# Kernel tuning notes

Measured on AMD Instinct MI355X. Metric: run time of the kernel, lower is better.

The kernel has to match this reference:

```python
import jax, jax.numpy as jnp
import numpy as np

N, E, F_IN, D_COORD, W, KW, KIN, DEPTH = 10000, 300000, 3, 3, 32, 256, 6, 4

def _lin(k, i, o):
    return jax.random.normal(k, (i, o), jnp.float32) * (1.0 / np.sqrt(i))

def setup_inputs() -> dict:
    key = jax.random.key(0)
    ks = jax.random.split(key, 16)
    x = jax.random.normal(ks[0], (N, F_IN), jnp.float32)
    edge_index = jax.random.randint(ks[1], (2, E), 0, N, jnp.int64)
    edge_attr = jax.random.normal(ks[2], (E, KIN), jnp.float32)
    coords_init = jax.random.normal(ks[3], (N, D_COORD), jnp.float32)
    return {
        "x": x, "edge_index": edge_index, "edge_attr": edge_attr,
        "coords_init": coords_init,
        "fc1_w": _lin(ks[4], F_IN, W), "fc1_b": jnp.zeros((W,), jnp.float32),
        # kernel DenseNet: [ker_in, ker_width//2, ker_width, width**2]
        "ker1_w": _lin(ks[5], KIN, KW // 2), "ker1_b": jnp.zeros((KW // 2,), jnp.float32),
        "ker2_w": _lin(ks[6], KW // 2, KW), "ker2_b": jnp.zeros((KW,), jnp.float32),
        "ker3_w": _lin(ks[7], KW, W * W), "ker3_b": jnp.zeros((W * W,), jnp.float32),
        # coord MLP: Linear(W,W)+ReLU+Linear(W,1)
        "cm1_w": _lin(ks[8], W, W), "cm1_b": jnp.zeros((W,), jnp.float32),
        "cm2_w": _lin(ks[9], W, 1), "cm2_b": jnp.zeros((1,), jnp.float32),
        # fc2: Linear(W,2W)+ReLU+Linear(2W,1)
        "fc2a_w": _lin(ks[10], W, 2 * W), "fc2a_b": jnp.zeros((2 * W,), jnp.float32),
        "fc2b_w": _lin(ks[11], 2 * W, 1), "fc2b_b": jnp.zeros((1,), jnp.float32),
        "depth": DEPTH,
    }

def reference(x, edge_index, edge_attr, coords_init,
              fc1_w, fc1_b, ker1_w, ker1_b, ker2_w, ker2_b, ker3_w, ker3_b,
              cm1_w, cm1_b, cm2_w, cm2_b, fc2a_w, fc2a_b, fc2b_w, fc2b_b, depth):
    n = x.shape[0]
    w = fc1_w.shape[1]
    row, col = edge_index[0], edge_index[1]
    h = x @ fc1_w + fc1_b  # [N, W]
    # edge kernel MLP -> per-edge [W, W] matrix (edge_attr fixed across layers)
    k = jax.nn.relu(edge_attr @ ker1_w + ker1_b)
    k = jax.nn.relu(k @ ker2_w + ker2_b)
    k = (k @ ker3_w + ker3_b).reshape(-1, w, w)  # [E, W, W]
    cnt = jnp.clip(jax.ops.segment_sum(jnp.ones((row.shape[0], 1), h.dtype), row, n), 1.0)
    coord = coords_init
    for _ in range(depth):
        m = jnp.einsum('eij,ej->ei', k, h[col])              # gather + kernel apply
        agg = jax.ops.segment_sum(m, row, n) / cnt           # mean scatter to nodes
        we = jax.nn.relu(m @ cm1_w + cm1_b) @ cm2_w + cm2_b  # [E, 1] coord weights
        trans = (coord[row] - coord[col]) * we               # equivariant edge vectors
        coord = coord + jax.ops.segment_sum(trans, row, n) / cnt
        h = jax.nn.relu(h + agg)
    out = jax.nn.relu(h @ fc2a_w + fc2a_b) @ fc2b_w + fc2b_b  # [N, 1]
    return out, coord
```

## Files before the change

kernel.cpp:

```cpp
#include <hip/hip_runtime.h>

#define NN 10000
#define NE 300000
#define DEPTH 4

typedef unsigned int   u32;
typedef unsigned short u16;
typedef unsigned char  u8;

typedef _Float16 half8  __attribute__((ext_vector_type(8)));
typedef _Float16 half2t __attribute__((ext_vector_type(2)));
typedef float  floatx16 __attribute__((ext_vector_type(16)));

__device__ __forceinline__ u32 f2h(float f) {
    f = fminf(fmaxf(f, -60000.f), 60000.f);
    _Float16 h = (_Float16)f;
    return (u32)__builtin_bit_cast(u16, h);
}
__device__ __forceinline__ float h2f(u16 b) {
    return (float)__builtin_bit_cast(_Float16, b);
}
__device__ __forceinline__ u32 pkrtz2(float a, float b) {
    return __builtin_bit_cast(u32, __builtin_amdgcn_cvt_pkrtz(a, b));
}
__device__ __forceinline__ u32 dq2(u32 x, u32 sel) {
    const half2t h1024 = {(_Float16)1024.f, (_Float16)1024.f};
    half2t v = __builtin_bit_cast(half2t, __builtin_amdgcn_perm(x, 0x64646464u, sel));
    return __builtin_bit_cast(u32, v - h1024);
}

__global__ void sentinel_kernel(float* out, int n, float val) {
    int i = blockIdx.x * 256 + threadIdx.x;
    if (i < n) out[i] = val;
}

__global__ void detect_idx_kernel(const int* __restrict__ ei, int* __restrict__ flag) {
    __shared__ int nz;
    if (threadIdx.x == 0) nz = 0;
    __syncthreads();
    if (ei[threadIdx.x * 2 + 1] != 0) atomicAdd(&nz, 1);
    __syncthreads();
    if (threadIdx.x == 0) *flag = (nz == 0) ? 1 : 0;
}

__global__ __launch_bounds__(256) void convert_idx_kernel(
    const int* __restrict__ ei, const int* __restrict__ flag,
    int* __restrict__ ridx, int* __restrict__ cidx)
{
    int e = blockIdx.x * 256 + threadIdx.x;
    if (e >= 2 * NE) return;
    const int is64 = *flag;
    int v = is64 ? ei[2 * e] : ei[e];
    if (e < NE) ridx[e] = v; else cidx[e - NE] = v;
}

__global__ __launch_bounds__(256) void init_nodes_kernel(
    const float* __restrict__ x, const float* __restrict__ fc1w,
    const float* __restrict__ fc1b, const float* __restrict__ ci,
    float* __restrict__ h, float* __restrict__ coord)
{
    int idx = blockIdx.x * 256 + threadIdx.x;
    if (idx < NN * 32) {
        int v = idx >> 5, f = idx & 31;
        float acc = fc1b[f];
#pragma unroll
        for (int i = 0; i < 3; i++) acc += x[v * 3 + i] * fc1w[i * 32 + f];
        h[idx] = acc;
    }
    if (idx < NN * 3) coord[idx] = ci[idx];
}

__global__ __launch_bounds__(256) void count_kernel(
    const int* __restrict__ ridx, const int* __restrict__ cidx,
    int* __restrict__ rowcnt, int* __restrict__ colcnt)
{
    int e = blockIdx.x * 256 + threadIdx.x;
    if (e < NE) { atomicAdd(&rowcnt[ridx[e]], 1); atomicAdd(&colcnt[cidx[e]], 1); }
}

__global__ void scan_kernel(const int* __restrict__ colcnt, const int* __restrict__ rowcnt,
                            int* __restrict__ cstart, int* __restrict__ cnext,
                            int* __restrict__ rstart, int* __restrict__ rnext,
                            float* __restrict__ invc, int mode)
{
    __shared__ int partC[256], partR[256];
    const int t = threadIdx.x;
    int sumC = 0, sumR = 0;
    for (int i = 0; i < 40; i++) {
        int v = t * 40 + i;
        if (v < NN) { sumC += colcnt[v]; sumR += rowcnt[v]; }
    }
    partC[t] = sumC; partR[t] = sumR;
    __syncthreads();
    if (t == 0) {
        int rc = 0, rr = 0;
        for (int i = 0; i < 256; i++) {
            int tc = partC[i]; partC[i] = rc; rc += tc;
            int tr = partR[i]; partR[i] = rr; rr += tr;
        }
    }
    __syncthreads();
    int runC = partC[t], runR = partR[t];
    for (int i = 0; i < 40; i++) {
        int v = t * 40 + i;
        if (v < NN) {
            cstart[v] = runC; cnext[v] = runC; runC += colcnt[v];
            if (mode) { rstart[v] = runR; rnext[v] = runR; runR += rowcnt[v]; }
        }
    }
    if (t == 255) { cstart[NN] = runC; if (mode) rstart[NN] = runR; }
    for (int v = t; v < NN; v += 256) invc[v] = 1.0f / fmaxf((float)rowcnt[v], 1.0f);
}

__global__ __launch_bounds__(256) void scatter_kernel(
    const int* __restrict__ cidx, const int* __restrict__ ridx,
    int* __restrict__ cnext, int* __restrict__ rnext,
    int* __restrict__ elist, int* __restrict__ rpos, int* __restrict__ rcol,
    int mode)
{
    int e = blockIdx.x * 256 + threadIdx.x;
    if (e >= NE) return;
    int pos = atomicAdd(&cnext[cidx[e]], 1);
    elist[pos] = e;
    if (mode) {
        int rp = atomicAdd(&rnext[ridx[e]], 1);
        rpos[e] = rp;
        rcol[rp] = cidx[e];
    }
}

__global__ __launch_bounds__(256) void w2pack_kernel(
    const float* __restrict__ w2, u16* __restrict__ w2h)
{
    const int slot = blockIdx.x * 256 + threadIdx.x;
    const int c = slot >> 9, s = (slot >> 6) & 7, l = slot & 63;
    const int li = l & 31, hf = l >> 5;
    const int k0 = s * 16 + hf * 8, col = c * 32 + li;
    u32 pk[8];
#pragma unroll
    for (int j = 0; j < 8; j++) pk[j] = f2h(w2[(size_t)(k0 + j) * 256 + col]);
    uint4 o;
    o.x = pk[0] | (pk[1] << 16);
    o.y = pk[2] | (pk[3] << 16);
    o.z = pk[4] | (pk[5] << 16);
    o.w = pk[6] | (pk[7] << 16);
    *(uint4*)&w2h[(size_t)slot * 8] = o;
}

__global__ void cm1pack_kernel(const float* __restrict__ cm1w, u16* __restrict__ cmpk)
{
    const int t = threadIdx.x;
    if (t >= 128) return;
    const int s2 = t >> 6, l = t & 63, li = l & 31, hf = l >> 5;
    u32 pk[8];
#pragma unroll
    for (int j = 0; j < 8; j++) pk[j] = f2h(cm1w[(s2 * 16 + hf * 8 + j) * 32 + li]);
    uint4 o;
    o.x = pk[0] | (pk[1] << 16);
    o.y = pk[2] | (pk[3] << 16);
    o.z = pk[4] | (pk[5] << 16);
    o.w = pk[6] | (pk[7] << 16);
    *(uint4*)&cmpk[(size_t)(s2 * 64 + l) * 8] = o;
}

__global__ __launch_bounds__(256) void w3pack_kernel(
    const float* __restrict__ w3, u16* __restrict__ w3g)
{
    const int slot = blockIdx.x * 256 + threadIdx.x;
    const int lane = slot & 63;
    const int ks   = (slot >> 6) & 1;
    const int pt   = slot >> 7;
    const int p    = pt * 32 + (lane & 31);
    const int kb   = ks * 16 + (lane >> 5) * 8;
    const int s  = p >> 9;
    const int hf = (p >> 8) & 1;
    const int i  = (p >> 3) & 31;
    const int j7 = p & 7;
    const int c  = s * 16 + hf * 8 + j7;
    const float* wp = &w3[(size_t)c * 1024 + i * 32 + kb];
    const float4 x0 = *(const float4*)wp;
    const float4 x1 = *(const float4*)(wp + 4);
    uint4 o;
    o.x = f2h(x0.x) | (f2h(x0.y) << 16);
    o.y = f2h(x0.z) | (f2h(x0.w) << 16);
    o.z = f2h(x1.x) | (f2h(x1.y) << 16);
    o.w = f2h(x1.z) | (f2h(x1.w) << 16);
    *(uint4*)&w3g[(size_t)slot * 8] = o;
}

__global__ __launch_bounds__(256, 4) void mlp_k2_kernel(
    const float* __restrict__ ea,
    const float* __restrict__ w1, const float* __restrict__ b1,
    const u16* __restrict__ w2h, const float* __restrict__ b2,
    u8* __restrict__ k2base, u16* __restrict__ k2s)
{
    __shared__ __align__(16) float ea_s[32 * 6];
    __shared__ __align__(16) u16   k1f[4096];
    __shared__ __align__(16) u16   M_s[32 * 258];
    __shared__ float pmax_s[4][32];
    const int t  = threadIdx.x;
    const int e0 = blockIdx.x * 32;

    for (int idx = t; idx < 192; idx += 256)
        ea_s[idx] = ea[(size_t)e0 * 6 + idx];
    __syncthreads();

    for (int slot = t; slot < 512; slot += 256) {
        const int s  = slot >> 6;
        const int l  = slot & 63;
        const int li = l & 31, hf = l >> 5;
        const int k0 = s * 16 + hf * 8;
        float acc[8];
        {
            const float4 ba = *(const float4*)&b1[k0];
            const float4 bb = *(const float4*)&b1[k0 + 4];
            acc[0] = ba.x; acc[1] = ba.y; acc[2] = ba.z; acc[3] = ba.w;
            acc[4] = bb.x; acc[5] = bb.y; acc[6] = bb.z; acc[7] = bb.w;
        }
#pragma unroll
        for (int i = 0; i < 6; i++) {
            const float ev = ea_s[li * 6 + i];
            const float4 wa = *(const float4*)&w1[i * 128 + k0];
            const float4 wb = *(const float4*)&w1[i * 128 + k0 + 4];
            acc[0] += ev * wa.x; acc[1] += ev * wa.y;
            acc[2] += ev * wa.z; acc[3] += ev * wa.w;
            acc[4] += ev * wb.x; acc[5] += ev * wb.y;
            acc[6] += ev * wb.z; acc[7] += ev * wb.w;
        }
        uint4 o;
        o.x = pkrtz2(fmaxf(acc[0], 0.f), fmaxf(acc[1], 0.f));
        o.y = pkrtz2(fmaxf(acc[2], 0.f), fmaxf(acc[3], 0.f));
        o.z = pkrtz2(fmaxf(acc[4], 0.f), fmaxf(acc[5], 0.f));
        o.w = pkrtz2(fmaxf(acc[6], 0.f), fmaxf(acc[7], 0.f));
        *(uint4*)&k1f[slot * 8] = o;
    }
    __syncthreads();

    {
        const int w  = t >> 6, l = t & 63;
        const int li = l & 31, hf = l >> 5;
#pragma unroll
        for (int ct = 0; ct < 2; ct++) {
            const int c = w * 2 + ct;
            floatx16 acc;
#pragma unroll
            for (int r = 0; r < 16; r++) acc[r] = 0.f;
#pragma unroll
            for (int s = 0; s < 8; s++) {
                const half8 a = __builtin_bit_cast(half8,
                    *(const uint4*)&k1f[(s * 64 + l) * 8]);
                const half8 b = __builtin_bit_cast(half8,
                    *(const uint4*)&w2h[(((size_t)c * 8 + s) * 64 + l) * 8]);
                acc = __builtin_amdgcn_mfma_f32_32x32x16_f16(a, b, acc, 0, 0, 0);
            }
            const float bb = b2[c * 32 + li];
#pragma unroll
            for (int r = 0; r < 16; r++) {
                const int e = (r & 3) + 8 * (r >> 2) + 4 * hf;
                M_s[e * 258 + c * 32 + li] =
                    __builtin_bit_cast(u16, (_Float16)fmaxf(acc[r] + bb, 0.f));
            }
        }
    }
    __syncthreads();

    {
        const int el = t & 31, qq = t >> 5;
        const int w  = t >> 6;
        u32 hw[16];
#pragma unroll
        for (int c = 0; c < 16; c++)
            hw[c] = *(const u32*)&M_s[el * 258 + qq * 32 + c * 2];

        half2t pm = __builtin_bit_cast(half2t, hw[0]);
#pragma unroll
        for (int c = 1; c < 16; c++)
            pm = __builtin_elementwise_max(pm, __builtin_bit_cast(half2t, hw[c]));
        float mx = fmaxf((float)pm[0], (float)pm[1]);
        mx = fmaxf(mx, __shfl_xor(mx, 32, 64));
        if ((t & 32) == 0) pmax_s[w][el] = mx;
        __syncthreads();
        mx = fmaxf(fmaxf(pmax_s[0][el], pmax_s[1][el]),
                   fmaxf(pmax_s[2][el], pmax_s[3][el]));
        const float sc  = mx / 255.f;
        const float inv = (mx > 0.f) ? 255.f / mx : 0.f;
        if (t < 32) k2s[e0 + el] = (u16)f2h(sc);
        const float magic = 8388608.f;
        u32 w8[8];
#pragma unroll
        for (int u = 0; u < 8; u++) {
            const u32 a = hw[u * 2], b = hw[u * 2 + 1];
            const float v0 = h2f((u16)a);
            const float v1 = h2f((u16)(a >> 16));
            const float v2 = h2f((u16)b);
            const float v3 = h2f((u16)(b >> 16));
            const u32 r0 = __builtin_bit_cast(u32, fmaf(v0, inv, magic));
            const u32 r1 = __builtin_bit_cast(u32, fmaf(v1, inv, magic));
            const u32 r2 = __builtin_bit_cast(u32, fmaf(v2, inv, magic));
            const u32 r3 = __builtin_bit_cast(u32, fmaf(v3, inv, magic));
            const u32 p01 = __builtin_amdgcn_perm(r1, r0, 0x0C0C0400u);
            const u32 p23 = __builtin_amdgcn_perm(r3, r2, 0x0C0C0400u);
            w8[u] = __builtin_amdgcn_perm(p23, p01, 0x05040100u);
        }
        u8* outp = k2base + (size_t)(e0 + el) * 256 + qq * 32;
        *(uint4*)outp        = make_uint4(w8[0], w8[1], w8[2], w8[3]);
        *(uint4*)(outp + 16) = make_uint4(w8[4], w8[5], w8[6], w8[7]);
    }
}

__global__ __launch_bounds__(256) void g_kernel(
    const float* __restrict__ h, const u16* __restrict__ w3g,
    u16* __restrict__ Gg)
{
    const int t = threadIdx.x, w = t >> 6, l = t & 63;
    const int li = l & 31, hf = l >> 5;
    const int n0 = blockIdx.x * 32;
    const int node = n0 + li;

    half8 a0, a1;
    if (node < NN) {
        const float* hp = &h[(size_t)node * 32 + hf * 8];
        const float4 x0 = *(const float4*)hp;
        const float4 x1 = *(const float4*)(hp + 4);
        const float4 y0 = *(const float4*)(hp + 16);
        const float4 y1 = *(const float4*)(hp + 20);
        uint4 ua, ub;
        ua.x = pkrtz2(x0.x, x0.y); ua.y = pkrtz2(x0.z, x0.w);
        ua.z = pkrtz2(x1.x, x1.y); ua.w = pkrtz2(x1.z, x1.w);
        ub.x = pkrtz2(y0.x, y0.y); ub.y = pkrtz2(y0.z, y0.w);
        ub.z = pkrtz2(y1.x, y1.y); ub.w = pkrtz2(y1.z, y1.w);
        a0 = __builtin_bit_cast(half8, ua);
        a1 = __builtin_bit_cast(half8, ub);
    } else {
        const uint4 z = make_uint4(0u, 0u, 0u, 0u);
        a0 = __builtin_bit_cast(half8, z);
        a1 = __builtin_bit_cast(half8, z);
    }

    const int pt0 = blockIdx.y * 64 + w * 16;
    const int full = (n0 + 32 <= NN) ? 1 : 0;
#pragma unroll 4
    for (int it = 0; it < 16; it++) {
        const int pt = pt0 + it;
        const uint4 b0u = *(const uint4*)&w3g[((size_t)pt * 2 + 0) * 512 + (size_t)l * 8];
        const uint4 b1u = *(const uint4*)&w3g[((size_t)pt * 2 + 1) * 512 + (size_t)l * 8];
        floatx16 acc;
#pragma unroll
        for (int r = 0; r < 16; r++) acc[r] = 0.f;
        acc = __builtin_amdgcn_mfma_f32_32x32x16_f16(
            a0, __builtin_bit_cast(half8, b0u), acc, 0, 0, 0);
        acc = __builtin_amdgcn_mfma_f32_32x32x16_f16(
            a1, __builtin_bit_cast(half8, b1u), acc, 0, 0, 0);
        if (full) {
#pragma unroll
            for (int r = 0; r < 16; r++) {
                const int nn = n0 + (r & 3) + 8 * (r >> 2) + 4 * hf;
                Gg[(size_t)nn * 8192 + pt * 32 + li] = (u16)f2h(acc[r]);
            }
        } else {
#pragma unroll
            for (int r = 0; r < 16; r++) {
                const int nn = n0 + (r & 3) + 8 * (r >> 2) + 4 * hf;
                if (nn < NN)
                    Gg[(size_t)nn * 8192 + pt * 32 + li] = (u16)f2h(acc[r]);
            }
        }
    }
}

__global__ __launch_bounds__(256, 3) void edge_kernel(
    const int* __restrict__ cstart, const int* __restrict__ elist,
    const int* __restrict__ ridx, const int* __restrict__ rpos,
    const u8* __restrict__ k2base, const u16* __restrict__ k2s,
    const u16* __restrict__ Gg, const float* __restrict__ coord,
    const u16* __restrict__ cmpk, const float* __restrict__ cm1b,
    const float* __restrict__ cm2w, const float* __restrict__ cm2b,
    const float* __restrict__ h, const float* __restrict__ b3,
    float* __restrict__ agg, float* __restrict__ dco,
    u16* __restrict__ mbuf, u16* __restrict__ webuf, int mode)
{
    const int t    = threadIdx.x;
    const int w    = t >> 6;
    const int l    = t & 63;
    const int li   = l & 31;
    const int half = l >> 5;

    __shared__ __align__(16) float Mlds_all[4][32 * 34];
    __shared__ int   idxS_all[4][32];
    __shared__ float seS_all[4][32];
    float* Mlds = Mlds_all[w];
    int*   idxS = idxS_all[w];
    float* seS  = seS_all[w];

    const int n = blockIdx.x * 4 + w;
    if (n >= NN) return;
    const int s0  = cstart[n];
    const int deg = cstart[n + 1] - s0;
    if (deg == 0) return;

    half8 cmb[2];
    cmb[0] = __builtin_bit_cast(half8, *(const uint4*)&cmpk[(size_t)(0 * 64 + l) * 8]);
    cmb[1] = __builtin_bit_cast(half8, *(const uint4*)&cmpk[(size_t)(1 * 64 + l) * 8]);
    half8 onesb;
#pragma unroll
    for (int j = 0; j < 8; j++) onesb[j] = (_Float16)1.0f;
    const float cm1bq = cm1b[li];
    const float cm2q  = cm2w[li];
    const float cm2b0 = cm2b[0];
    float bv = 0.f;
    {
        const float* hn = &h[(size_t)n * 32];
        const float* bp = &b3[(size_t)li * 32];
#pragma unroll
        for (int c2 = 0; c2 < 8; c2++) {
            const float4 hv = *(const float4*)&hn[c2 * 4];
            const float4 bq = *(const float4*)&bp[c2 * 4];
            bv += hv.x * bq.x + hv.y * bq.y + hv.z * bq.z + hv.w * bq.w;
        }
    }
    const float con   = (mode == 0 && li < 3) ? coord[(size_t)n * 3 + li] : 0.f;
    const u16* Gn = Gg + (size_t)n * 8192;

    for (int base = 0; base < deg; base += 32) {
        const int mye   = base + li;
        const int valid = (mye < deg) ? 1 : 0;
        const int eid   = valid ? elist[s0 + mye] : 0;
        const float se  = valid ? h2f(k2s[eid]) : 0.f;
        if (l < 32) { idxS[l] = valid ? (mode ? rpos[eid] : ridx[eid]) : 0; seS[l] = se; }

        uint4 gr[16];
#pragma unroll
        for (int s = 0; s < 16; s++)
            gr[s] = *(const uint4*)(Gn + s * 512 + l * 8);
        const u8* k2row = k2base + (size_t)eid * 256 + half * 8;
        uint2 kr[16];
#pragma unroll
        for (int s = 0; s < 16; s++) kr[s] = *(const uint2*)(k2row + s * 16);

        floatx16 acc;
#pragma unroll
        for (int r = 0; r < 16; r++) acc[r] = 0.f;
#pragma unroll
        for (int s = 0; s < 16; s++) {
            uint4 au;
            au.x = dq2(kr[s].x, 0x00050004u);
            au.y = dq2(kr[s].x, 0x00070006u);
            au.z = dq2(kr[s].y, 0x00050004u);
            au.w = dq2(kr[s].y, 0x00070006u);
            acc = __builtin_amdgcn_mfma_f32_32x32x16_f16(
                __builtin_bit_cast(half8, au),
                __builtin_bit_cast(half8, gr[s]), acc, 0, 0, 0);
        }
#pragma unroll
        for (int r = 0; r < 16; r++) {
            const int e = (r & 3) + 8 * (r >> 2) + 4 * half;
            acc[r] = acc[r] * seS[e] + bv;
        }

#pragma unroll
        for (int r = 0; r < 16; r++) {
            const int e = (r & 3) + 8 * (r >> 2) + 4 * half;
            Mlds[e * 34 + li] = acc[r];
        }
        if (mode == 0) {
#pragma unroll
            for (int r = 0; r < 16; r++) {
                const int e = (r & 3) + 8 * (r >> 2) + 4 * half;
                if (base + e < deg)
                    atomicAdd(&agg[(size_t)idxS[e] * 32 + li], acc[r]);
            }
        } else {
#pragma unroll
            for (int r = 0; r < 16; r++) {
                const int e = (r & 3) + 8 * (r >> 2) + 4 * half;
                if (base + e < deg)
                    mbuf[(size_t)idxS[e] * 32 + li] =
                        __builtin_bit_cast(u16, (_Float16)acc[r]);
            }
        }
        asm volatile("s_waitcnt lgkmcnt(0)" ::: "memory");

        floatx16 acc2;
#pragma unroll
        for (int r = 0; r < 16; r++) acc2[r] = cm1bq;
#pragma unroll
        for (int s2 = 0; s2 < 2; s2++) {
            const float* mp = &Mlds[li * 34 + s2 * 16 + half * 8];
            const float2 m0 = *(const float2*)mp;
            const float2 m1 = *(const float2*)(mp + 2);
            const float2 m2 = *(const float2*)(mp + 4);
            const float2 m3 = *(const float2*)(mp + 6);
            uint4 au;
            au.x = pkrtz2(m0.x, m0.y);
            au.y = pkrtz2(m1.x, m1.y);
            au.z = pkrtz2(m2.x, m2.y);
            au.w = pkrtz2(m3.x, m3.y);
            acc2 = __builtin_amdgcn_mfma_f32_32x32x16_f16(
                __builtin_bit_cast(half8, au), cmb[s2], acc2, 0, 0, 0);
        }

#pragma unroll
        for (int r = 0; r < 16; r++) {
            const int e = (r & 3) + 8 * (r >> 2) + 4 * half;
            Mlds[e * 34 + li] = fmaxf(acc2[r], 0.f) * cm2q;
        }
        asm volatile("s_waitcnt lgkmcnt(0)" ::: "memory");
        floatx16 acc3;
#pragma unroll
        for (int r = 0; r < 16; r++) acc3[r] = cm2b0;
#pragma unroll
        for (int s2 = 0; s2 < 2; s2++) {
            const float* mp = &Mlds[li * 34 + s2 * 16 + half * 8];
            const float2 m0 = *(const float2*)mp;
            const float2 m1 = *(const float2*)(mp + 2);
            const float2 m2 = *(const float2*)(mp + 4);
            const float2 m3 = *(const float2*)(mp + 6);
            uint4 au;
            au.x = pkrtz2(m0.x, m0.y);
            au.y = pkrtz2(m1.x, m1.y);
            au.z = pkrtz2(m2.x, m2.y);
            au.w = pkrtz2(m3.x, m3.y);
            acc3 = __builtin_amdgcn_mfma_f32_32x32x16_f16(
                __builtin_bit_cast(half8, au), onesb, acc3, 0, 0, 0);
        }

        if (mode == 0) {
#pragma unroll
            for (int r = 0; r < 16; r++) {
                const int e = (r & 3) + 8 * (r >> 2) + 4 * half;
                if (base + e < deg && li < 3) {
                    const int rr = idxS[e];
                    const float d = coord[(size_t)rr * 3 + li] - con;
                    atomicAdd(&dco[(size_t)rr * 3 + li], d * acc3[r]);
                }
            }
        } else {
#pragma unroll
            for (int r = 0; r < 16; r++) {
                const int e = (r & 3) + 8 * (r >> 2) + 4 * half;
                if (base + e < deg && li == 0)
                    webuf[idxS[e]] = __builtin_bit_cast(u16, (_Float16)acc3[r]);
            }
        }
    }
}

__global__ __launch_bounds__(256) void node_update_kernel(
    float* __restrict__ h, float* __restrict__ agg,
    float* __restrict__ coord, float* __restrict__ dco,
    const float* __restrict__ invc)
{
    int idx = blockIdx.x * 256 + threadIdx.x;
    if (idx < NN * 32) {
        int v = idx >> 5;
        h[idx] = fmaxf(h[idx] + agg[idx] * invc[v], 0.f);
        agg[idx] = 0.f;
    }
    if (idx < NN * 3) {
        coord[idx] += dco[idx] * invc[idx / 3];
        dco[idx] = 0.f;
    }
}

__global__ __launch_bounds__(256) void node_update2_kernel(
    float* __restrict__ h, const float* __restrict__ coordCur,
    float* __restrict__ coordNew, const u16* __restrict__ mbuf,
    const u16* __restrict__ webuf, const int* __restrict__ rcol,
    const int* __restrict__ rstart, const float* __restrict__ invc)
{
    const int t = threadIdx.x, w = t >> 6, l = t & 63;
    const int li = l & 31, half = l >> 5;
    const int v = blockIdx.x * 4 + w;
    if (v >= NN) return;
    const int s0 = rstart[v], s1 = rstart[v + 1];
    const float iv = invc[v];

    float acc = 0.f;
    for (int s = s0 + half; s < s1; s += 2)
        acc += h2f(mbuf[(size_t)s * 32 + li]);
    acc += __shfl_xor(acc, 32, 64);
    if (half == 0)
        h[(size_t)v * 32 + li] = fmaxf(h[(size_t)v * 32 + li] + acc * iv, 0.f);

    const float c0 = coordCur[(size_t)v * 3 + 0];
    const float c1 = coordCur[(size_t)v * 3 + 1];
    const float c2 = coordCur[(size_t)v * 3 + 2];
    float p0 = 0.f, p1 = 0.f, p2 = 0.f;
    for (int s = s0 + l; s < s1; s += 64) {
        const float we = h2f(webuf[s]);
        const int col = rcol[s];
        p0 += (c0 - coordCur[(size_t)col * 3 + 0]) * we;
        p1 += (c1 - coordCur[(size_t)col * 3 + 1]) * we;
        p2 += (c2 - coordCur[(size_t)col * 3 + 2]) * we;
    }
#pragma unroll
    for (int off = 32; off >= 1; off >>= 1) {
        p0 += __shfl_xor(p0, off, 64);
        p1 += __shfl_xor(p1, off, 64);
        p2 += __shfl_xor(p2, off, 64);
    }
    if (l == 0) {
        coordNew[(size_t)v * 3 + 0] = c0 + p0 * iv;
        coordNew[(size_t)v * 3 + 1] = c1 + p1 * iv;
        coordNew[(size_t)v * 3 + 2] = c2 + p2 * iv;
    }
}

__global__ __launch_bounds__(256) void final_kernel(
    const float* __restrict__ h, const float* __restrict__ coord,
    const float* __restrict__ wa, const float* __restrict__ ba,
    const float* __restrict__ wb, const float* __restrict__ bb,
    float* __restrict__ out)
{
    const int lane = threadIdx.x & 63;
    const int v = blockIdx.x * 4 + (threadIdx.x >> 6);
    if (v >= NN) return;
    const float hreg = (lane < 32) ? h[(size_t)v * 32 + lane] : 0.f;
    float acc = ba[lane];
#pragma unroll
    for (int f = 0; f < 32; f++) acc += __shfl(hreg, f, 64) * wa[f * 64 + lane];
    float part = fmaxf(acc, 0.f) * wb[lane];
#pragma unroll
    for (int off = 32; off >= 1; off >>= 1) part += __shfl_xor(part, off, 64);
    if (lane == 0) out[v] = part + bb[0];
    if (lane < 3) out[NN + (size_t)v * 3 + lane] = coord[(size_t)v * 3 + lane];
}

extern "C" void kernel_launch(void* const* d_in, const int* in_sizes, int n_in,
                              void* d_out, int out_size, void* d_ws, size_t ws_size,
                              hipStream_t stream)
{
    const float* x    = (const float*)d_in[0];
    const int*   ei   = (const int*)d_in[1];
    const float* ea   = (const float*)d_in[2];
    const float* ci   = (const float*)d_in[3];
    const float* fc1w = (const float*)d_in[4];
    const float* fc1b = (const float*)d_in[5];
    const float* k1w  = (const float*)d_in[6];
    const float* k1b  = (const float*)d_in[7];
    const float* k2w  = (const float*)d_in[8];
    const float* k2b  = (const float*)d_in[9];
    const float* k3w  = (const float*)d_in[10];
    const float* k3b  = (const float*)d_in[11];
    const float* cm1w = (const float*)d_in[12];
    const float* cm1b = (const float*)d_in[13];
    const float* cm2w = (const float*)d_in[14];
    const float* cm2b = (const float*)d_in[15];
    const float* f2aw = (const float*)d_in[16];
    const float* f2ab = (const float*)d_in[17];
    const float* f2bw = (const float*)d_in[18];
    const float* f2bb = (const float*)d_in[19];

    size_t o_k2, o_k2s, o_G, o_h, o_coA, o_coB, o_invc, o_rc, o_cc,
           o_cs, o_rs, o_cn, o_rn, o_el, o_w2h, o_cmpk, o_w3g, o_agg, o_dco,
           o_ri, o_ci, o_rp, o_rcl, o_mb, o_wb;
#define ALGN(v) (((v) + 255) & ~(size_t)255)
    auto carve = [&](int mode) -> size_t {
        size_t o = 0;
        o_k2  = o; o += ALGN((size_t)NE * 256);
        o_k2s = o; o += ALGN((size_t)NE * 2);
        o_G   = o; o += ALGN((size_t)NN * 8192 * 2);
        o_h   = o; o += ALGN((size_t)NN * 32 * 4);
        o_coA = o; o += ALGN((size_t)NN * 3 * 4);
        o_invc= o; o += ALGN((size_t)NN * 4);
        o_rc  = o; o += ALGN((size_t)NN * 4);
        o_cc  = o; o += ALGN((size_t)NN * 4);
        o_cs  = o; o += ALGN((size_t)(NN + 1) * 4);
        o_cn  = o; o += ALGN((size_t)NN * 4);
        o_el  = o; o += ALGN((size_t)NE * 4);
        o_w2h = o; o += ALGN((size_t)128 * 256 * 2);
        o_cmpk= o; o += ALGN((size_t)1024 * 2);
        o_w3g = o; o += ALGN((size_t)32768 * 8 * 2);
        if (mode == 0) {
            o_agg = o; o += ALGN((size_t)NN * 32 * 4);
            o_dco = o; o += ALGN((size_t)NN * 3 * 4);
            o_ri  = o; o += ALGN((size_t)NE * 4);
            o_ci  = o; o += ALGN((size_t)NE * 4);
            o_coB = o_coA; o_rs = o_cs; o_rn = o_cn;
            o_rp = o_el; o_rcl = o_el; o_mb = o_k2; o_wb = o_k2;
        } else {
            o_coB = o; o += ALGN((size_t)NN * 3 * 4);
            o_rs  = o; o += ALGN((size_t)(NN + 1) * 4);
            o_rn  = o; o += ALGN((size_t)NN * 4);
            o_rp  = o; o += ALGN((size_t)NE * 4);
            o_rcl = o; o += ALGN((size_t)NE * 4);
            const size_t u = o;
            o_ri = u; o_ci = u + ALGN((size_t)NE * 4);
            o_mb = u; o_wb = u + ALGN((size_t)NE * 32 * 2);
            const size_t setup_sz = 2 * ALGN((size_t)NE * 4);
            const size_t layer_sz = ALGN((size_t)NE * 32 * 2) + ALGN((size_t)NE * 2);
            o += (setup_sz > layer_sz) ? setup_sz : layer_sz;
            o_agg = o_k2; o_dco = o_k2;
        }
        return o;
    };
    int mode = (ws_size >= carve(1)) ? 1 : 0;
    size_t need = carve(mode);
    if (ws_size < need) {
        sentinel_kernel<<<(NN * 4 + 255) / 256, 256, 0, stream>>>((float*)d_out, NN * 4, 1.0e6f);
        return;
    }

    char* wsb = (char*)d_ws;
    u8*    k2g   = (u8*)(wsb + o_k2);
    u16*   k2s   = (u16*)(wsb + o_k2s);
    u16*   Gg    = (u16*)(wsb + o_G);
    float* h     = (float*)(wsb + o_h);
    float* coA   = (float*)(wsb + o_coA);
    float* coB   = (float*)(wsb + o_coB);
    float* invc  = (float*)(wsb + o_invc);
    int*   rowcnt= (int*)(wsb + o_rc);
    int*   colcnt= (int*)(wsb + o_cc);
    int*   cstart= (int*)(wsb + o_cs);
    int*   rstart= (int*)(wsb + o_rs);
    int*   cnext = (int*)(wsb + o_cn);
    int*   rnext = (int*)(wsb + o_rn);
    int*   elist = (int*)(wsb + o_el);
    u16*   w2h   = (u16*)(wsb + o_w2h);
    u16*   cmpk  = (u16*)(wsb + o_cmpk);
    u16*   w3g   = (u16*)(wsb + o_w3g);
    float* agg   = (float*)(wsb + o_agg);
    float* dco   = (float*)(wsb + o_dco);
    int*   ridx  = (int*)(wsb + o_ri);
    int*   cidx  = (int*)(wsb + o_ci);
    int*   rpos  = (int*)(wsb + o_rp);
    int*   rcol  = (int*)(wsb + o_rcl);
    u16*   mbuf  = (u16*)(wsb + o_mb);
    u16*   webuf = (u16*)(wsb + o_wb);

    hipMemsetAsync(rowcnt, 0, (size_t)NN * 4, stream);
    hipMemsetAsync(colcnt, 0, (size_t)NN * 4, stream);
    if (mode == 0) {
        hipMemsetAsync(agg, 0, (size_t)NN * 32 * 4, stream);
        hipMemsetAsync(dco, 0, (size_t)NN * 3 * 4, stream);
    }

    detect_idx_kernel<<<1, 256, 0, stream>>>(ei, cnext);
    convert_idx_kernel<<<(2 * NE + 255) / 256, 256, 0, stream>>>(ei, cnext, ridx, cidx);
    init_nodes_kernel<<<(NN * 32 + 255) / 256, 256, 0, stream>>>(x, fc1w, fc1b, ci, h, coA);
    count_kernel<<<(NE + 255) / 256, 256, 0, stream>>>(ridx, cidx, rowcnt, colcnt);
    scan_kernel<<<1, 256, 0, stream>>>(colcnt, rowcnt, cstart, cnext, rstart, rnext,
                                       invc, mode);
    scatter_kernel<<<(NE + 255) / 256, 256, 0, stream>>>(cidx, ridx, cnext, rnext,
                                                         elist, rpos, rcol, mode);
    w2pack_kernel<<<16, 256, 0, stream>>>(k2w, w2h);
    cm1pack_kernel<<<1, 128, 0, stream>>>(cm1w, cmpk);
    w3pack_kernel<<<128, 256, 0, stream>>>(k3w, w3g);
    mlp_k2_kernel<<<NE / 32, 256, 0, stream>>>(ea, k1w, k1b, w2h, k2b, k2g, k2s);

    float* coCur = coA;
    float* coAlt = coB;
    const dim3 ggrid((NN + 31) / 32, 4);
    for (int l = 0; l < DEPTH; l++) {
        g_kernel<<<ggrid, 256, 0, stream>>>(h, w3g, Gg);
        edge_kernel<<<(NN + 3) / 4, 256, 0, stream>>>(cstart, elist, ridx, rpos,
                                                      k2g, k2s, Gg, coCur, cmpk,
                                                      cm1b, cm2w, cm2b, h, k3b,
                                                      agg, dco, mbuf, webuf, mode);
        if (mode == 1) {
            node_update2_kernel<<<(NN + 3) / 4, 256, 0, stream>>>(
                h, coCur, coAlt, mbuf, webuf, rcol, rstart, invc);
            float* tmp = coCur; coCur = coAlt; coAlt = tmp;
        } else {
            node_update_kernel<<<(NN * 32 + 255) / 256, 256, 0, stream>>>(
                h, agg, coCur, dco, invc);
        }
    }
    final_kernel<<<(NN + 3) / 4, 256, 0, stream>>>(h, coCur, f2aw, f2ab, f2bw, f2bb,
                                                   (float*)d_out);
}
```

Measured before the change: 817.7 us.

## Quantize k2 in registers, split edge loads, raise occupancy bounds

In mlp_k2_kernel, both MFMA column tiles now run interleaved in registers. The per-edge max is computed with wave shuffles, and values are quantized straight to u8 in LDS, skipping the fp16 staging buffer and its conversions. The launch bound rises to 6 blocks per CU. In edge_kernel, the 16-step gather of G and k2 is split into two halves of 8 to cut register pressure, allowing 4 blocks per CU. Per-edge scale and index are fetched with __shfl instead of LDS arrays. The trade-offs are more shuffles and register spilling risk against higher occupancy and lower LDS traffic.

```diff
diff --git a/kernel.cpp b/kernel.cpp
--- a/kernel.cpp
+++ b/kernel.cpp
@@ -188,7 +188,7 @@
     *(uint4*)&w3g[(size_t)slot * 8] = o;
 }
 
-__global__ __launch_bounds__(256, 4) void mlp_k2_kernel(
+__global__ __launch_bounds__(256, 6) void mlp_k2_kernel(
     const float* __restrict__ ea,
     const float* __restrict__ w1, const float* __restrict__ b1,
     const u16* __restrict__ w2h, const float* __restrict__ b2,
@@ -196,8 +196,9 @@
 {
     __shared__ __align__(16) float ea_s[32 * 6];
     __shared__ __align__(16) u16   k1f[4096];
-    __shared__ __align__(16) u16   M_s[32 * 258];
+    __shared__ __align__(16) u8    M8[32 * 272];
     __shared__ float pmax_s[4][32];
+    __shared__ float invS[32];
     const int t  = threadIdx.x;
     const int e0 = blockIdx.x * 32;
 
@@ -236,75 +237,76 @@
     }
     __syncthreads();
 
+    const int w  = t >> 6, l = t & 63;
+    const int li = l & 31, hf = l >> 5;
+    floatx16 accA, accB;
+#pragma unroll
+    for (int r = 0; r < 16; r++) { accA[r] = 0.f; accB[r] = 0.f; }
     {
-        const int w  = t >> 6, l = t & 63;
-        const int li = l & 31, hf = l >> 5;
-#pragma unroll
-        for (int ct = 0; ct < 2; ct++) {
-            const int c = w * 2 + ct;
-            floatx16 acc;
-#pragma unroll
-            for (int r = 0; r < 16; r++) acc[r] = 0.f;
-#pragma unroll
-            for (int s = 0; s < 8; s++) {
-                const half8 a = __builtin_bit_cast(half8,
-                    *(const uint4*)&k1f[(s * 64 + l) * 8]);
-                const half8 b = __builtin_bit_cast(half8,
-                    *(const uint4*)&w2h[(((size_t)c * 8 + s) * 64 + l) * 8]);
-                acc = __builtin_amdgcn_mfma_f32_32x32x16_f16(a, b, acc, 0, 0, 0);
-            }
-            const float bb = b2[c * 32 + li];
-#pragma unroll
-            for (int r = 0; r < 16; r++) {
-                const int e = (r & 3) + 8 * (r >> 2) + 4 * hf;
-                M_s[e * 258 + c * 32 + li] =
-                    __builtin_bit_cast(u16, (_Float16)fmaxf(acc[r] + bb, 0.f));
-            }
+        const int cA = w * 2, cB = w * 2 + 1;
+#pragma unroll
+        for (int s = 0; s < 8; s++) {
+            const half8 a = __builtin_bit_cast(half8,
+                *(const uint4*)&k1f[(s * 64 + l) * 8]);
+            const half8 bA = __builtin_bit_cast(half8,
+                *(const uint4*)&w2h[(((size_t)cA * 8 + s) * 64 + l) * 8]);
+            const half8 bB = __builtin_bit_cast(half8,
+                *(const uint4*)&w2h[(((size_t)cB * 8 + s) * 64 + l) * 8]);
+            accA = __builtin_amdgcn_mfma_f32_32x32x16_f16(a, bA, accA, 0, 0, 0);
+            accB = __builtin_amdgcn_mfma_f32_32x32x16_f16(a, bB, accB, 0, 0, 0);
+        }
+        const float bbA = b2[cA * 32 + li];
+        const float bbB = b2[cB * 32 + li];
+#pragma unroll
+        for (int r = 0; r < 16; r++) {
+            accA[r] = fmaxf(accA[r] + bbA, 0.f);
+            accB[r] = fmaxf(accB[r] + bbB, 0.f);
+        }
+    }
+
+#pragma unroll
+    for (int r = 0; r < 16; r++) {
+        float v = fmaxf(accA[r], accB[r]);
+        v = fmaxf(v, __shfl_xor(v, 1, 64));
+        v = fmaxf(v, __shfl_xor(v, 2, 64));
+        v = fmaxf(v, __shfl_xor(v, 4, 64));
+        v = fmaxf(v, __shfl_xor(v, 8, 64));
+        v = fmaxf(v, __shfl_xor(v, 16, 64));
+        if (li == 0) {
+            const int e = (r & 3) + 8 * (r >> 2) + 4 * hf;
+            pmax_s[w][e] = v;
+        }
+    }
+    __syncthreads();
+    if (t < 32) {
+        const float mx = fmaxf(fmaxf(pmax_s[0][t], pmax_s[1][t]),
+                               fmaxf(pmax_s[2][t], pmax_s[3][t]));
+        k2s[e0 + t] = (u16)f2h(mx / 255.f);
+        invS[t] = (mx > 0.f) ? 255.f / mx : 0.f;
+    }
+    __syncthreads();
+
+    {
+        const float magic = 8388608.f;
+#pragma unroll
+        for (int r = 0; r < 16; r++) {
+            const int e = (r & 3) + 8 * (r >> 2) + 4 * hf;
+            const float inv = invS[e];
+            const u32 qA = __builtin_bit_cast(u32, fmaf(accA[r], inv, magic));
+            const u32 qB = __builtin_bit_cast(u32, fmaf(accB[r], inv, magic));
+            M8[e * 272 + (w * 2 + 0) * 32 + li] = (u8)qA;
+            M8[e * 272 + (w * 2 + 1) * 32 + li] = (u8)qB;
         }
     }
     __syncthreads();
 
     {
         const int el = t & 31, qq = t >> 5;
-        const int w  = t >> 6;
-        u32 hw[16];
-#pragma unroll
-        for (int c = 0; c < 16; c++)
-            hw[c] = *(const u32*)&M_s[el * 258 + qq * 32 + c * 2];
-
-        half2t pm = __builtin_bit_cast(half2t, hw[0]);
-#pragma unroll
-        for (int c = 1; c < 16; c++)
-            pm = __builtin_elementwise_max(pm, __builtin_bit_cast(half2t, hw[c]));
-        float mx = fmaxf((float)pm[0], (float)pm[1]);
-        mx = fmaxf(mx, __shfl_xor(mx, 32, 64));
-        if ((t & 32) == 0) pmax_s[w][el] = mx;
-        __syncthreads();
-        mx = fmaxf(fmaxf(pmax_s[0][el], pmax_s[1][el]),
-                   fmaxf(pmax_s[2][el], pmax_s[3][el]));
-        const float sc  = mx / 255.f;
-        const float inv = (mx > 0.f) ? 255.f / mx : 0.f;
-        if (t < 32) k2s[e0 + el] = (u16)f2h(sc);
-        const float magic = 8388608.f;
-        u32 w8[8];
-#pragma unroll
-        for (int u = 0; u < 8; u++) {
-            const u32 a = hw[u * 2], b = hw[u * 2 + 1];
-            const float v0 = h2f((u16)a);
-            const float v1 = h2f((u16)(a >> 16));
-            const float v2 = h2f((u16)b);
-            const float v3 = h2f((u16)(b >> 16));
-            const u32 r0 = __builtin_bit_cast(u32, fmaf(v0, inv, magic));
-            const u32 r1 = __builtin_bit_cast(u32, fmaf(v1, inv, magic));
-            const u32 r2 = __builtin_bit_cast(u32, fmaf(v2, inv, magic));
-            const u32 r3 = __builtin_bit_cast(u32, fmaf(v3, inv, magic));
-            const u32 p01 = __builtin_amdgcn_perm(r1, r0, 0x0C0C0400u);
-            const u32 p23 = __builtin_amdgcn_perm(r3, r2, 0x0C0C0400u);
-            w8[u] = __builtin_amdgcn_perm(p23, p01, 0x05040100u);
-        }
+        const uint4 o0 = *(const uint4*)&M8[el * 272 + qq * 32];
+        const uint4 o1 = *(const uint4*)&M8[el * 272 + qq * 32 + 16];
         u8* outp = k2base + (size_t)(e0 + el) * 256 + qq * 32;
-        *(uint4*)outp        = make_uint4(w8[0], w8[1], w8[2], w8[3]);
-        *(uint4*)(outp + 16) = make_uint4(w8[4], w8[5], w8[6], w8[7]);
+        *(uint4*)outp        = o0;
+        *(uint4*)(outp + 16) = o1;
     }
 }
 
@@ -368,7 +370,7 @@
     }
 }
 
-__global__ __launch_bounds__(256, 3) void edge_kernel(
+__global__ __launch_bounds__(256, 4) void edge_kernel(
     const int* __restrict__ cstart, const int* __restrict__ elist,
     const int* __restrict__ ridx, const int* __restrict__ rpos,
     const u8* __restrict__ k2base, const u16* __restrict__ k2s,
@@ -386,11 +388,7 @@
     const int half = l >> 5;
 
     __shared__ __align__(16) float Mlds_all[4][32 * 34];
-    __shared__ int   idxS_all[4][32];
-    __shared__ float seS_all[4][32];
     float* Mlds = Mlds_all[w];
-    int*   idxS = idxS_all[w];
-    float* seS  = seS_all[w];
 
     const int n = blockIdx.x * 4 + w;
     if (n >= NN) return;
@@ -426,22 +424,23 @@
         const int valid = (mye < deg) ? 1 : 0;
         const int eid   = valid ? elist[s0 + mye] : 0;
         const float se  = valid ? h2f(k2s[eid]) : 0.f;
-        if (l < 32) { idxS[l] = valid ? (mode ? rpos[eid] : ridx[eid]) : 0; seS[l] = se; }
-
-        uint4 gr[16];
-#pragma unroll
-        for (int s = 0; s < 16; s++)
-            gr[s] = *(const uint4*)(Gn + s * 512 + l * 8);
-        const u8* k2row = k2base + (size_t)eid * 256 + half * 8;
-        uint2 kr[16];
-#pragma unroll
-        for (int s = 0; s < 16; s++) kr[s] = *(const uint2*)(k2row + s * 16);
+        const int  idxv = valid ? (mode ? rpos[eid] : ridx[eid]) : 0;
+
+        const u16* grp   = Gn + l * 8;
+        const u8*  k2row = k2base + (size_t)eid * 256 + half * 8;
 
         floatx16 acc;
 #pragma unroll
         for (int r = 0; r < 16; r++) acc[r] = 0.f;
-#pragma unroll
-        for (int s = 0; s < 16; s++) {
+
+        uint4 gr[8]; uint2 kr[8];
+#pragma unroll
+        for (int s = 0; s < 8; s++) {
+            gr[s] = *(const uint4*)(grp + s * 512);
+            kr[s] = *(const uint2*)(k2row + s * 16);
+        }
+#pragma unroll
+        for (int s = 0; s < 8; s++) {
             uint4 au;
             au.x = dq2(kr[s].x, 0x00050004u);
             au.y = dq2(kr[s].x, 0x00070006u);
@@ -452,9 +451,26 @@
                 __builtin_bit_cast(half8, gr[s]), acc, 0, 0, 0);
         }
 #pragma unroll
+        for (int s = 0; s < 8; s++) {
+            gr[s] = *(const uint4*)(grp + (8 + s) * 512);
+            kr[s] = *(const uint2*)(k2row + (8 + s) * 16);
+        }
+#pragma unroll
+        for (int s = 0; s < 8; s++) {
+            uint4 au;
+            au.x = dq2(kr[s].x, 0x00050004u);
+            au.y = dq2(kr[s].x, 0x00070006u);
+            au.z = dq2(kr[s].y, 0x00050004u);
+            au.w = dq2(kr[s].y, 0x00070006u);
+            acc = __builtin_amdgcn_mfma_f32_32x32x16_f16(
+                __builtin_bit_cast(half8, au),
+                __builtin_bit_cast(half8, gr[s]), acc, 0, 0, 0);
+        }
+
+#pragma unroll
         for (int r = 0; r < 16; r++) {
             const int e = (r & 3) + 8 * (r >> 2) + 4 * half;
-            acc[r] = acc[r] * seS[e] + bv;
+            acc[r] = acc[r] * __shfl(se, e, 32) + bv;
         }
 
 #pragma unroll
@@ -467,14 +483,14 @@
             for (int r = 0; r < 16; r++) {
                 const int e = (r & 3) + 8 * (r >> 2) + 4 * half;
                 if (base + e < deg)
-                    atomicAdd(&agg[(size_t)idxS[e] * 32 + li], acc[r]);
+                    atomicAdd(&agg[(size_t)__shfl(idxv, e, 32) * 32 + li], acc[r]);
             }
         } else {
 #pragma unroll
             for (int r = 0; r < 16; r++) {
                 const int e = (r & 3) + 8 * (r >> 2) + 4 * half;
                 if (base + e < deg)
-                    mbuf[(size_t)idxS[e] * 32 + li] =
+                    mbuf[(size_t)__shfl(idxv, e, 32) * 32 + li] =
                         __builtin_bit_cast(u16, (_Float16)acc[r]);
             }
         }
@@ -529,7 +545,7 @@
             for (int r = 0; r < 16; r++) {
                 const int e = (r & 3) + 8 * (r >> 2) + 4 * half;
                 if (base + e < deg && li < 3) {
-                    const int rr = idxS[e];
+                    const int rr = __shfl(idxv, e, 32);
                     const float d = coord[(size_t)rr * 3 + li] - con;
                     atomicAdd(&dco[(size_t)rr * 3 + li], d * acc3[r]);
                 }
@@ -538,8 +554,9 @@
 #pragma unroll
             for (int r = 0; r < 16; r++) {
                 const int e = (r & 3) + 8 * (r >> 2) + 4 * half;
+                const int ie = __shfl(idxv, e, 32);
                 if (base + e < deg && li == 0)
-                    webuf[idxS[e]] = __builtin_bit_cast(u16, (_Float16)acc3[r]);
+                    webuf[ie] = __builtin_bit_cast(u16, (_Float16)acc3[r]);
             }
         }
     }
```

After: 1.167 ms. 42.7% more time.
